# Performance work log

Measured on AMD Instinct MI355X. Metric: run time of the kernel, lower is better.

## Reference

```python
import jax, jax.numpy as jnp
import numpy as np
from functools import partial


def edt_sq(mask):
    """Exact squared Euclidean distance transform (distance from True pixels to
    nearest False pixel), separable two-pass algorithm. mask: bool (..., H, W).
    Matches scipy.ndimage.distance_transform_edt(mask)**2 whenever each 2-D
    slice contains at least one background (False) pixel."""
    H, W = mask.shape[-2], mask.shape[-1]
    LARGE = jnp.float32(H * H + W * W + 1)

    # ---- pass 1: 1-D distance to nearest False along H (rows axis) ----
    mm = jnp.moveaxis(mask, -2, 0)  # (H, ..., W)
    init = jnp.full(mm.shape[1:], LARGE, dtype=jnp.float32)

    def step1(carry, x):
        d = jnp.where(x, carry + 1.0, 0.0)
        return d, d

    _, fwd = jax.lax.scan(step1, init, mm)
    _, bwd = jax.lax.scan(step1, init, mm[::-1])
    d1 = jnp.minimum(fwd, bwd[::-1])            # (H, ..., W) 1-D distance
    f = jnp.minimum(d1 * d1, LARGE)             # squared, capped
    f = jnp.moveaxis(f, 0, -2)                  # (..., H, W)

    # ---- pass 2: D[..., j] = min_k f[..., k] + (j - k)^2 along W ----
    j = jnp.arange(W, dtype=jnp.float32)
    fT = jnp.moveaxis(f, -1, 0)                 # (W, ..., H)

    def step2(D, xk):
        fk, k = xk                               # fk: (..., H)
        cand = fk[..., None] + (j - k) ** 2      # (..., H, W)
        return jnp.minimum(D, cand), None

    D0 = jnp.full(f.shape, LARGE, dtype=jnp.float32)
    D, _ = jax.lax.scan(step2, D0, (fT, j))
    return D


def setup_inputs() -> dict:
    key = jax.random.key(0)
    k1, k2 = jax.random.split(key)
    output = jax.random.normal(k1, (16, 2, 512, 512), dtype=jnp.float32)
    target = jax.random.randint(k2, (16, 512, 512), 0, 2).astype(jnp.int64)
    return {"output": output, "target": target}


def reference(output, target):
    B, C, H, W = output.shape
    probs = jax.nn.softmax(output, axis=1)                    # (B,C,H,W)
    y_onehot = jax.nn.one_hot(target, C, axis=1, dtype=jnp.float32)

    # distance maps only needed for channels 1: (loop starts at c=1)
    pc_mask = probs[:, 1:] > 0.5                              # (B,C-1,H,W)
    gt_mask = y_onehot[:, 1:] > 0.5
    pc_dist_sq = edt_sq(pc_mask)
    gt_dist_sq = edt_sq(gt_mask)
    dist = jax.lax.stop_gradient(pc_dist_sq + gt_dist_sq)     # no_grad in torch

    pred_error = (probs - y_onehot) ** 2                      # (B,C,H,W)
    multipled = pred_error[:, 1:] * dist                      # einsum 'bcxy,bcxy->bcxy'
    return multipled.mean()
```

## Files before the change

### kernel.cpp

```cpp
#include <hip/hip_runtime.h>

#define BB   16
#define HH   512
#define WW   512
#define HWSZ (HH * WW)
#define NPIX (BB * HWSZ)
#define LARGE_F 524289.0f
#define WT 16
#define NW 16
#define NLOSSBLK (BB * HH / 2)

__device__ __forceinline__ int colprobe(const unsigned int* __restrict__ bits,
                                        int c, int i, int sel) {
  int w = i >> 5, bp = i & 31;
  int cb = c * (NW + 1) * 2 + sel;
  unsigned cur = bits[cb + w * 2];
  unsigned zu = ~cur & (0xFFFFFFFFu >> (31 - bp));
  unsigned zd = ~cur & (0xFFFFFFFFu << bp);
  int up = 0xFFFF, dn = 0xFFFF;
  if (zu) {
    up = bp - (31 - __clz(zu));
  } else {
    for (int ww = w - 1; ww >= 0; --ww) {
      unsigned z = ~bits[cb + ww * 2];
      if (z) { up = i - (ww * 32 + 31 - __clz(z)); break; }
    }
  }
  if (zd) {
    dn = (__ffs(zd) - 1) - bp;
  } else {
    for (int ww = w + 1; ww < NW; ++ww) {
      unsigned z = ~bits[cb + ww * 2];
      if (z) { dn = ww * 32 + (__ffs(z) - 1) - i; break; }
    }
  }
  int r = min(up, dn);
  return min(r, 0xFFFF);
}

__global__ __launch_bounds__(512) void coldist_kernel(
    const float* __restrict__ out4,
    const int* __restrict__ target,
    unsigned int* __restrict__ cr) {
  __shared__ unsigned char mbyte[HH * WT];
  __shared__ unsigned int bits[WT * (NW + 1) * 2];

  const int c0 = blockIdx.x * WT;
  const int b  = blockIdx.y;
  const float* ch0 = out4 + (size_t)(b * 2) * HWSZ;
  const float* ch1 = ch0 + HWSZ;
  const int* tb = target + (size_t)b * HWSZ;

#pragma unroll
  for (int s = 0; s < 4; ++s) {
    int m  = s * 512 + threadIdx.x;
    int i  = m >> 2;
    int cq = (m & 3) * 4;
    int g  = i * WW + c0 + cq;
    float4 a0 = *(const float4*)(ch0 + g);
    float4 a1 = *(const float4*)(ch1 + g);
    int4   t4 = *(const int4*)(tb + g);
    unsigned p = 0;
    p |= (unsigned)(((a1.x > a0.x) ? 1u : 0u) | ((t4.x == 1) ? 2u : 0u));
    p |= (unsigned)(((a1.y > a0.y) ? 1u : 0u) | ((t4.y == 1) ? 2u : 0u)) << 8;
    p |= (unsigned)(((a1.z > a0.z) ? 1u : 0u) | ((t4.z == 1) ? 2u : 0u)) << 16;
    p |= (unsigned)(((a1.w > a0.w) ? 1u : 0u) | ((t4.w == 1) ? 2u : 0u)) << 24;
    *(unsigned*)&mbyte[i * WT + cq] = p;
  }
  __syncthreads();

  if (threadIdx.x < 256) {
    int c = threadIdx.x >> 4;
    int w = threadIdx.x & 15;
    unsigned pcw = 0, gtw = 0;
    int base = w * 32 * WT + c;
#pragma unroll
    for (int k = 0; k < 32; ++k) {
      unsigned mb = mbyte[base + k * WT];
      pcw |= (mb & 1u) << k;
      gtw |= ((mb >> 1) & 1u) << k;
    }
    bits[(c * (NW + 1) + w) * 2]     = pcw;
    bits[(c * (NW + 1) + w) * 2 + 1] = gtw;
  }
  __syncthreads();

  unsigned int* crb = cr + (size_t)b * HWSZ;
#pragma unroll 1
  for (int s = 0; s < 16; ++s) {
    int p = s * 512 + threadIdx.x;
    int i = p >> 4;
    int c = p & 15;
    int rpc = colprobe(bits, c, i, 0);
    int rgt = colprobe(bits, c, i, 1);
    crb[i * WW + c0 + c] = (unsigned)rpc | ((unsigned)rgt << 16);
  }
}

__global__ __launch_bounds__(512) void loss_kernel(
    const float* __restrict__ out4,
    const unsigned int* __restrict__ cr,
    float* __restrict__ partials) {
  __shared__ float2 f0[WW];
  __shared__ float2 f1[WW];
  __shared__ float ssum[8];

  const int b  = blockIdx.x >> 8;
  const int i0 = (blockIdx.x & 255) * 2;
  const int j  = threadIdx.x;
  const size_t base = (size_t)b * HWSZ + (size_t)i0 * WW;

  unsigned v0 = cr[base + j];
  unsigned v1 = cr[base + WW + j];
  const float* xp = out4 + (size_t)(b * 2) * HWSZ + (size_t)i0 * WW;
  float x00 = xp[j], x01 = xp[WW + j];
  float x10 = xp[HWSZ + j], x11 = xp[HWSZ + WW + j];

  unsigned rp0 = v0 & 0xFFFFu, rg0 = v0 >> 16;
  unsigned rp1 = v1 & 0xFFFFu, rg1 = v1 >> 16;
  float fpc0 = (rp0 >= 512) ? LARGE_F : (float)(rp0 * rp0);
  float fgt0 = (rg0 >= 512) ? LARGE_F : (float)(rg0 * rg0);
  float fpc1 = (rp1 >= 512) ? LARGE_F : (float)(rp1 * rp1);
  float fgt1 = (rg1 >= 512) ? LARGE_F : (float)(rg1 * rg1);
  f0[j] = make_float2(fpc0, fgt0);
  f1[j] = make_float2(fpc1, fgt1);
  __syncthreads();

  float bpc0 = fpc0, bgt0 = fgt0, bpc1 = fpc1, bgt1 = fgt1;
  for (int r = 1; r < WW; ++r) {
    float rr = (float)(r * r);
    if (rr >= bpc0 && rr >= bgt0 && rr >= bpc1 && rr >= bgt1) break;
    int jl = j - r, jr = j + r;
    if (jl >= 0) {
      float2 a = f0[jl], c2 = f1[jl];
      bpc0 = fminf(bpc0, a.x + rr);  bgt0 = fminf(bgt0, a.y + rr);
      bpc1 = fminf(bpc1, c2.x + rr); bgt1 = fminf(bgt1, c2.y + rr);
    }
    if (jr < WW) {
      float2 a = f0[jr], c2 = f1[jr];
      bpc0 = fminf(bpc0, a.x + rr);  bgt0 = fminf(bgt0, a.y + rr);
      bpc1 = fminf(bpc1, c2.x + rr); bgt1 = fminf(bgt1, c2.y + rr);
    }
  }

  float p10 = 1.0f / (1.0f + expf(x00 - x10));
  float p11 = 1.0f / (1.0f + expf(x01 - x11));
  float y10 = (rg0 != 0) ? 1.0f : 0.0f;
  float y11 = (rg1 != 0) ? 1.0f : 0.0f;
  float d0 = p10 - y10, d1 = p11 - y11;
  float contrib = (d0 * d0 * (bpc0 + bgt0) + d1 * d1 * (bpc1 + bgt1))
                  * (1.0f / (float)NPIX);

  for (int off = 32; off > 0; off >>= 1) contrib += __shfl_down(contrib, off);
  int lane = threadIdx.x & 63;
  int wave = threadIdx.x >> 6;
  if (lane == 0) ssum[wave] = contrib;
  __syncthreads();
  if (threadIdx.x == 0) {
    float s = 0.0f;
#pragma unroll
    for (int w = 0; w < 8; ++w) s += ssum[w];
    partials[blockIdx.x] = s;
  }
}

__global__ __launch_bounds__(1024) void reduce_kernel(
    const float* __restrict__ partials, float* __restrict__ d_out) {
  __shared__ float ssum[16];
  float s = 0.0f;
#pragma unroll
  for (int k = 0; k < NLOSSBLK / 1024; ++k)
    s += partials[k * 1024 + threadIdx.x];
  for (int off = 32; off > 0; off >>= 1) s += __shfl_down(s, off);
  int lane = threadIdx.x & 63;
  int wave = threadIdx.x >> 6;
  if (lane == 0) ssum[wave] = s;
  __syncthreads();
  if (threadIdx.x == 0) {
    float t = 0.0f;
#pragma unroll
    for (int w = 0; w < 16; ++w) t += ssum[w];
    *d_out = t;
  }
}

extern "C" void kernel_launch(void* const* d_in, const int* in_sizes, int n_in,
                              void* d_out, int out_size, void* d_ws, size_t ws_size,
                              hipStream_t stream) {
  const float* out4 = (const float*)d_in[0];
  const int* target = (const int*)d_in[1];
  unsigned int* cr = (unsigned int*)d_ws;
  float* partials = (float*)(cr + NPIX);
  float* out = (float*)d_out;

  dim3 grid1(WW / WT, BB);
  coldist_kernel<<<grid1, 512, 0, stream>>>(out4, target, cr);

  loss_kernel<<<NLOSSBLK, 512, 0, stream>>>(out4, cr, partials);

  reduce_kernel<<<1, 1024, 0, stream>>>(partials, out);
}
```

Before: 112.4 us.

## Pack column bitmasks globally and compute column distances inside loss kernel

The first kernel now writes only packed 32-row bit words per column to global memory instead of a full per-pixel 32-bit column-distance map. This cuts intermediate traffic from about 16M words to about 0.5M words. The loss kernel loads a window of nearby bit words into shared memory and runs the column probe itself, falling back to global reads for distant words. Each block now handles four rows instead of two, which spreads the horizontal min search and its early-exit check across more rows per block. In exchange, the early exit waits for the slowest of four rows, and shared memory use rises, which could lower occupancy.

```diff
diff --git a/kernel.cpp b/kernel.cpp
--- a/kernel.cpp
+++ b/kernel.cpp
@@ -6,57 +6,31 @@
 #define HWSZ (HH * WW)
 #define NPIX (BB * HWSZ)
 #define LARGE_F 524289.0f
-#define WT 16
 #define NW 16
-#define NLOSSBLK (BB * HH / 2)
-
-__device__ __forceinline__ int colprobe(const unsigned int* __restrict__ bits,
-                                        int c, int i, int sel) {
-  int w = i >> 5, bp = i & 31;
-  int cb = c * (NW + 1) * 2 + sel;
-  unsigned cur = bits[cb + w * 2];
-  unsigned zu = ~cur & (0xFFFFFFFFu >> (31 - bp));
-  unsigned zd = ~cur & (0xFFFFFFFFu << bp);
-  int up = 0xFFFF, dn = 0xFFFF;
-  if (zu) {
-    up = bp - (31 - __clz(zu));
-  } else {
-    for (int ww = w - 1; ww >= 0; --ww) {
-      unsigned z = ~bits[cb + ww * 2];
-      if (z) { up = i - (ww * 32 + 31 - __clz(z)); break; }
-    }
-  }
-  if (zd) {
-    dn = (__ffs(zd) - 1) - bp;
-  } else {
-    for (int ww = w + 1; ww < NW; ++ww) {
-      unsigned z = ~bits[cb + ww * 2];
-      if (z) { dn = ww * 32 + (__ffs(z) - 1) - i; break; }
-    }
-  }
-  int r = min(up, dn);
-  return min(r, 0xFFFF);
-}
-
-__global__ __launch_bounds__(512) void coldist_kernel(
+#define GR 4
+#define NLOSSBLK (BB * HH / GR)
+
+
+__global__ __launch_bounds__(512) void pack_kernel(
     const float* __restrict__ out4,
     const int* __restrict__ target,
-    unsigned int* __restrict__ cr) {
-  __shared__ unsigned char mbyte[HH * WT];
-  __shared__ unsigned int bits[WT * (NW + 1) * 2];
-
-  const int c0 = blockIdx.x * WT;
-  const int b  = blockIdx.y;
+    unsigned int* __restrict__ bitsG) {
+  __shared__ unsigned char mbyte[32 * 256];
+
+  const int w    = blockIdx.x >> 1;
+  const int half = blockIdx.x & 1;
+  const int b    = blockIdx.y;
+  const int c0   = half * 256;
   const float* ch0 = out4 + (size_t)(b * 2) * HWSZ;
   const float* ch1 = ch0 + HWSZ;
   const int* tb = target + (size_t)b * HWSZ;
 
 #pragma unroll
   for (int s = 0; s < 4; ++s) {
-    int m  = s * 512 + threadIdx.x;
-    int i  = m >> 2;
-    int cq = (m & 3) * 4;
-    int g  = i * WW + c0 + cq;
+    int q  = s * 512 + threadIdx.x;
+    int i  = q >> 6;
+    int cq = (q & 63) * 4;
+    int g  = (w * 32 + i) * WW + c0 + cq;
     float4 a0 = *(const float4*)(ch0 + g);
     float4 a1 = *(const float4*)(ch1 + g);
     int4   t4 = *(const int4*)(tb + g);
@@ -65,91 +39,134 @@
     p |= (unsigned)(((a1.y > a0.y) ? 1u : 0u) | ((t4.y == 1) ? 2u : 0u)) << 8;
     p |= (unsigned)(((a1.z > a0.z) ? 1u : 0u) | ((t4.z == 1) ? 2u : 0u)) << 16;
     p |= (unsigned)(((a1.w > a0.w) ? 1u : 0u) | ((t4.w == 1) ? 2u : 0u)) << 24;
-    *(unsigned*)&mbyte[i * WT + cq] = p;
-  }
-  __syncthreads();
-
-  if (threadIdx.x < 256) {
-    int c = threadIdx.x >> 4;
-    int w = threadIdx.x & 15;
-    unsigned pcw = 0, gtw = 0;
-    int base = w * 32 * WT + c;
+    *(unsigned*)&mbyte[i * 256 + cq] = p;
+  }
+  __syncthreads();
+
+  {
+    int c   = threadIdx.x & 255;
+    int sel = threadIdx.x >> 8;
+    unsigned wd = 0;
 #pragma unroll
     for (int k = 0; k < 32; ++k) {
-      unsigned mb = mbyte[base + k * WT];
-      pcw |= (mb & 1u) << k;
-      gtw |= ((mb >> 1) & 1u) << k;
-    }
-    bits[(c * (NW + 1) + w) * 2]     = pcw;
-    bits[(c * (NW + 1) + w) * 2 + 1] = gtw;
-  }
-  __syncthreads();
-
-  unsigned int* crb = cr + (size_t)b * HWSZ;
-#pragma unroll 1
-  for (int s = 0; s < 16; ++s) {
-    int p = s * 512 + threadIdx.x;
-    int i = p >> 4;
-    int c = p & 15;
-    int rpc = colprobe(bits, c, i, 0);
-    int rgt = colprobe(bits, c, i, 1);
-    crb[i * WW + c0 + c] = (unsigned)rpc | ((unsigned)rgt << 16);
-  }
+      unsigned mb = mbyte[k * 256 + c];
+      wd |= ((mb >> sel) & 1u) << k;
+    }
+    bitsG[(size_t)((b * 2 + sel) * NW + w) * WW + c0 + c] = wd;
+  }
+}
+
+__device__ __forceinline__ int colprobe(const unsigned (*lb)[WW],
+                                        const unsigned* __restrict__ gcol,
+                                        int wlo, int whi, int j, int i) {
+  int w = i >> 5, bp = i & 31;
+  unsigned cur = lb[w - wlo][j];
+  unsigned zu = ~cur & (0xFFFFFFFFu >> (31 - bp));
+  unsigned zd = ~cur & (0xFFFFFFFFu << bp);
+  int up = 0xFFFF, dn = 0xFFFF;
+  if (zu) {
+    up = bp - (31 - __clz(zu));
+  } else {
+    for (int ww = w - 1; ww >= 0; --ww) {
+      unsigned z = ~((ww >= wlo) ? lb[ww - wlo][j] : gcol[ww * WW]);
+      if (z) { up = i - (ww * 32 + 31 - __clz(z)); break; }
+    }
+  }
+  if (zd) {
+    dn = (__ffs((int)zd) - 1) - bp;
+  } else {
+    for (int ww = w + 1; ww < NW; ++ww) {
+      unsigned z = ~((ww <= whi) ? lb[ww - wlo][j] : gcol[ww * WW]);
+      if (z) { dn = ww * 32 + (__ffs((int)z) - 1) - i; break; }
+    }
+  }
+  return min(min(up, dn), 0xFFFF);
 }
 
 __global__ __launch_bounds__(512) void loss_kernel(
     const float* __restrict__ out4,
-    const unsigned int* __restrict__ cr,
+    const unsigned int* __restrict__ bitsG,
     float* __restrict__ partials) {
-  __shared__ float2 f0[WW];
-  __shared__ float2 f1[WW];
+  __shared__ unsigned lbits[2][5][WW];
+  __shared__ float2 fv[GR][WW];
   __shared__ float ssum[8];
 
-  const int b  = blockIdx.x >> 8;
-  const int i0 = (blockIdx.x & 255) * 2;
+  const int b  = blockIdx.x >> 7;
+  const int i0 = (blockIdx.x & 127) * GR;
   const int j  = threadIdx.x;
-  const size_t base = (size_t)b * HWSZ + (size_t)i0 * WW;
-
-  unsigned v0 = cr[base + j];
-  unsigned v1 = cr[base + WW + j];
+
+  const int wc  = i0 >> 5;
+  const int wlo = max(0, wc - 2);
+  const int whi = min(NW - 1, wc + 2);
+  const int nwr = whi - wlo + 1;
+
+  const unsigned* gb = bitsG + (size_t)(b * 2) * NW * WW;
+  for (int idx = threadIdx.x; idx < nwr * 2 * WW; idx += 512) {
+    int c    = idx & (WW - 1);
+    int rest = idx >> 9;
+    int wrel = rest >> 1;
+    int sel  = rest & 1;
+    lbits[sel][wrel][c] = gb[(size_t)(sel * NW + wlo + wrel) * WW + c];
+  }
+
   const float* xp = out4 + (size_t)(b * 2) * HWSZ + (size_t)i0 * WW;
-  float x00 = xp[j], x01 = xp[WW + j];
-  float x10 = xp[HWSZ + j], x11 = xp[HWSZ + WW + j];
-
-  unsigned rp0 = v0 & 0xFFFFu, rg0 = v0 >> 16;
-  unsigned rp1 = v1 & 0xFFFFu, rg1 = v1 >> 16;
-  float fpc0 = (rp0 >= 512) ? LARGE_F : (float)(rp0 * rp0);
-  float fgt0 = (rg0 >= 512) ? LARGE_F : (float)(rg0 * rg0);
-  float fpc1 = (rp1 >= 512) ? LARGE_F : (float)(rp1 * rp1);
-  float fgt1 = (rg1 >= 512) ? LARGE_F : (float)(rg1 * rg1);
-  f0[j] = make_float2(fpc0, fgt0);
-  f1[j] = make_float2(fpc1, fgt1);
-  __syncthreads();
-
-  float bpc0 = fpc0, bgt0 = fgt0, bpc1 = fpc1, bgt1 = fgt1;
+  float x0v[GR], x1v[GR];
+#pragma unroll
+  for (int rw = 0; rw < GR; ++rw) {
+    x0v[rw] = xp[rw * WW + j];
+    x1v[rw] = xp[HWSZ + rw * WW + j];
+  }
+  __syncthreads();
+
+  const unsigned* gpc = gb + j;
+  const unsigned* ggt = gb + NW * WW + j;
+  float y1v[GR];
+  float bpc[GR], bgt[GR];
+#pragma unroll
+  for (int rw = 0; rw < GR; ++rw) {
+    int i = i0 + rw;
+    int rpc = colprobe(lbits[0], gpc, wlo, whi, j, i);
+    int rgt = colprobe(lbits[1], ggt, wlo, whi, j, i);
+    float fpc = (rpc >= 512) ? LARGE_F : (float)(rpc * rpc);
+    float fgt = (rgt >= 512) ? LARGE_F : (float)(rgt * rgt);
+    fv[rw][j] = make_float2(fpc, fgt);
+    bpc[rw] = fpc; bgt[rw] = fgt;
+    y1v[rw] = (rgt != 0) ? 1.0f : 0.0f;
+  }
+  __syncthreads();
+
   for (int r = 1; r < WW; ++r) {
     float rr = (float)(r * r);
-    if (rr >= bpc0 && rr >= bgt0 && rr >= bpc1 && rr >= bgt1) break;
+    float mx = fmaxf(fmaxf(fmaxf(bpc[0], bgt[0]), fmaxf(bpc[1], bgt[1])),
+                     fmaxf(fmaxf(bpc[2], bgt[2]), fmaxf(bpc[3], bgt[3])));
+    if (rr >= mx) break;
     int jl = j - r, jr = j + r;
     if (jl >= 0) {
-      float2 a = f0[jl], c2 = f1[jl];
-      bpc0 = fminf(bpc0, a.x + rr);  bgt0 = fminf(bgt0, a.y + rr);
-      bpc1 = fminf(bpc1, c2.x + rr); bgt1 = fminf(bgt1, c2.y + rr);
+#pragma unroll
+      for (int rw = 0; rw < GR; ++rw) {
+        float2 a = fv[rw][jl];
+        bpc[rw] = fminf(bpc[rw], a.x + rr);
+        bgt[rw] = fminf(bgt[rw], a.y + rr);
+      }
     }
     if (jr < WW) {
-      float2 a = f0[jr], c2 = f1[jr];
-      bpc0 = fminf(bpc0, a.x + rr);  bgt0 = fminf(bgt0, a.y + rr);
-      bpc1 = fminf(bpc1, c2.x + rr); bgt1 = fminf(bgt1, c2.y + rr);
-    }
-  }
-
-  float p10 = 1.0f / (1.0f + expf(x00 - x10));
-  float p11 = 1.0f / (1.0f + expf(x01 - x11));
-  float y10 = (rg0 != 0) ? 1.0f : 0.0f;
-  float y11 = (rg1 != 0) ? 1.0f : 0.0f;
-  float d0 = p10 - y10, d1 = p11 - y11;
-  float contrib = (d0 * d0 * (bpc0 + bgt0) + d1 * d1 * (bpc1 + bgt1))
-                  * (1.0f / (float)NPIX);
+#pragma unroll
+      for (int rw = 0; rw < GR; ++rw) {
+        float2 a = fv[rw][jr];
+        bpc[rw] = fminf(bpc[rw], a.x + rr);
+        bgt[rw] = fminf(bgt[rw], a.y + rr);
+      }
+    }
+  }
+
+  float contrib = 0.0f;
+#pragma unroll
+  for (int rw = 0; rw < GR; ++rw) {
+    float p1 = 1.0f / (1.0f + expf(x0v[rw] - x1v[rw]));
+    float d = p1 - y1v[rw];
+    contrib += d * d * (bpc[rw] + bgt[rw]);
+  }
+  contrib *= (1.0f / (float)NPIX);
 
   for (int off = 32; off > 0; off >>= 1) contrib += __shfl_down(contrib, off);
   int lane = threadIdx.x & 63;
@@ -189,14 +206,14 @@
                               hipStream_t stream) {
   const float* out4 = (const float*)d_in[0];
   const int* target = (const int*)d_in[1];
-  unsigned int* cr = (unsigned int*)d_ws;
-  float* partials = (float*)(cr + NPIX);
+  unsigned int* bitsG = (unsigned int*)d_ws;
+  float* partials = (float*)(bitsG + BB * 2 * NW * WW);
   float* out = (float*)d_out;
 
-  dim3 grid1(WW / WT, BB);
-  coldist_kernel<<<grid1, 512, 0, stream>>>(out4, target, cr);
-
-  loss_kernel<<<NLOSSBLK, 512, 0, stream>>>(out4, cr, partials);
+  dim3 grid1(32, BB);
+  pack_kernel<<<grid1, 512, 0, stream>>>(out4, target, bitsG);
+
+  loss_kernel<<<NLOSSBLK, 512, 0, stream>>>(out4, bitsG, partials);
 
   reduce_kernel<<<1, 1024, 0, stream>>>(partials, out);
 }
```

Result: faster. 103.7 us (-7.8%).
